# Kernel tuning notes

Measured on AMD Instinct MI355X. Metric: run time of the kernel, lower is better.

The kernel has to match this reference:

```python
import jax, jax.numpy as jnp
import numpy as np

B, N, K = 8, 1024, 32
C_IN, C_OUT, C_SIPF, HEADS = 128, 256, 8, 4
D_H = C_IN // HEADS
EPS = 1e-5
NEG_SLOPE = 0.2


def setup_inputs() -> dict:
    key = jax.random.key(0)
    ks = jax.random.split(key, 12)
    s = 0.05
    x = jax.random.normal(ks[0], (B, C_IN, N), jnp.float32)
    SiPF = jax.random.normal(ks[1], (B, N, K, C_SIPF), jnp.float32)
    col_local = jax.random.randint(ks[2], (B, N, K), 0, N)
    # feat_select expects GLOBAL indices (it subtracts the b*N base)
    col = (col_local + jnp.arange(B)[:, None, None] * N).reshape(-1).astype(jnp.int64)
    return {
        "x": x,
        "SiPF": SiPF,
        "w_kv": jax.random.normal(ks[3], (2 * C_IN, C_IN), jnp.float32) * s,
        "wk1": jax.random.normal(ks[4], (C_IN, C_SIPF), jnp.float32) * s,
        "bnk_gamma": jnp.ones((C_IN,), jnp.float32),
        "bnk_beta": jnp.zeros((C_IN,), jnp.float32),
        "wk2": jax.random.normal(ks[5], (C_IN, C_IN), jnp.float32) * s,
        "wv1": jax.random.normal(ks[6], (C_IN, C_SIPF), jnp.float32) * s,
        "bv1": jnp.zeros((C_IN,), jnp.float32),
        "bnv_gamma": jnp.ones((C_IN,), jnp.float32),
        "bnv_beta": jnp.zeros((C_IN,), jnp.float32),
        "wv2": jax.random.normal(ks[7], (C_IN, C_IN), jnp.float32) * s,
        "bv2": jnp.zeros((C_IN,), jnp.float32),
        "we": jax.random.normal(ks[8], (C_OUT, 2 * C_IN), jnp.float32) * s,
        "bne_gamma": jnp.ones((C_OUT,), jnp.float32),
        "bne_beta": jnp.zeros((C_OUT,), jnp.float32),
        "col": col,
        "bs": B,
    }


def _bn2d(t, gamma, beta):
    # BatchNorm2d, training mode: stats over (B, N, K) per channel
    m = t.mean(axis=(0, 2, 3), keepdims=True)
    v = t.var(axis=(0, 2, 3), keepdims=True)
    return (t - m) * jax.lax.rsqrt(v + EPS) * gamma[None, :, None, None] + beta[None, :, None, None]


def _bn1d(t, gamma, beta):
    m = t.mean(axis=(0, 2), keepdims=True)
    v = t.var(axis=(0, 2), keepdims=True)
    return (t - m) * jax.lax.rsqrt(v + EPS) * gamma[None, :, None] + beta[None, :, None]


def _feat_select(feat, col):
    # feat: [B, C, N]; col: [B*N*K] global indices -> [B, C, N, K]
    idx = col.reshape(B, N * K) - (jnp.arange(B, dtype=col.dtype) * N)[:, None]
    gathered = jax.vmap(lambda f, i: f[:, i])(feat, idx)  # [B, C, N*K]
    return gathered.reshape(feat.shape[0], feat.shape[1], N, K)


def _forward(x, SiPF, col, w_kv, wk1, bnk_gamma, bnk_beta, wk2,
             wv1, bv1, bnv_gamma, bnv_beta, wv2, bv2, we, bne_gamma, bne_beta):
    fs = _feat_select(x, col)                               # [B, C_in, N, K]
    sipf = SiPF.reshape(B, N, K, C_SIPF).transpose(0, 3, 1, 2)  # [B, C_sipf, N, K]

    qv = jnp.einsum('oc,bcnk->bonk', w_kv, fs)
    q_fs, v_fs = qv[:, :C_IN], qv[:, C_IN:]

    # bias nets on SiPF (1x1 conv -> BN -> ReLU -> 1x1 conv)
    hk = jax.nn.relu(_bn2d(jnp.einsum('oc,bcnk->bonk', wk1, sipf), bnk_gamma, bnk_beta))
    k_sipf = jnp.einsum('oc,bcnk->bonk', wk2, hk)
    hv = jnp.einsum('oc,bcnk->bonk', wv1, sipf) + bv1[None, :, None, None]
    hv = jax.nn.relu(_bn2d(hv, bnv_gamma, bnv_beta))
    v_sipf = jnp.einsum('oc,bcnk->bonk', wv2, hv) + bv2[None, :, None, None]

    def to_heads(t):  # [B, C_in, N, K] -> [B, H, N, K, d_h]
        return t.reshape(B, HEADS, D_H, N, K).transpose(0, 1, 3, 4, 2)

    q = to_heads(q_fs)
    k = to_heads(k_sipf)
    v = to_heads(v_fs) * to_heads(v_sipf)

    scale = 1.0 / np.sqrt(D_H).astype(np.float32)
    scores = jnp.einsum('bhnkd,bhnjd->bhnkj', q, k) * scale   # [B, H, N, K, K]
    attn = jax.nn.softmax(scores, axis=-1)
    out = jnp.einsum('bhnkj,bhnjd->bhnkd', attn, v)           # [B, H, N, K, d_h]

    y = out.transpose(0, 1, 4, 2, 3).reshape(B, C_IN, N, K)
    y = y.max(axis=-1)                                        # [B, C_in, N]

    z = jnp.concatenate([y - x, x], axis=1)                   # [B, 2*C_in, N]
    z = jnp.einsum('oc,bcn->bon', we, z)
    z = _bn1d(z, bne_gamma, bne_beta)
    return jnp.where(z >= 0, z, NEG_SLOPE * z)                # LeakyReLU(0.2)


def reference(x, SiPF, w_kv, wk1, bnk_gamma, bnk_beta, wk2, wv1, bv1,
              bnv_gamma, bnv_beta, wv2, bv2, we, bne_gamma, bne_beta, col, bs):
    del bs  # unused by the torch module as well
    return _forward(x, SiPF, col, w_kv, wk1, bnk_gamma, bnk_beta, wk2,
                    wv1, bv1, bnv_gamma, bnv_beta, wv2, bv2, we, bne_gamma, bne_beta)
```

## Files before the change

### kernel.cpp

```cpp
#include <hip/hip_runtime.h>

#define B_    8
#define N_    1024
#define K_    32
#define CIN   128
#define COUT  256
#define EPSF  1e-5f
#define NEG   0.2f

#define WS_MP   0
#define WS_ESUM 12288
#define WS_ESS  12544
#define WS_BK   12800
#define WS_BV   12928
#define WB_BYTE 53248
#define XT_BYTE 331776
#define Y_BYTE  2428928
#define WQB   0
#define WVB   16384
#define WK2B  32768
#define WV2B  49152
#define WEB   65536
#define WK1F  131072
#define WV1F  135168

typedef unsigned short ushort_t;
typedef unsigned int   uint_t;
typedef __attribute__((ext_vector_type(8))) short s8v;
typedef __attribute__((ext_vector_type(4))) short s4v;
typedef __attribute__((ext_vector_type(4))) float f4v;
typedef __bf16 bf16x8 __attribute__((ext_vector_type(8)));

constexpr int   P_TOT  = B_ * N_ * K_;
constexpr float INV_P  = 1.0f / (float)P_TOT;
constexpr float INV_BN = 1.0f / (float)(B_ * N_);

__device__ __forceinline__ float b2f(ushort_t u) {
    return __uint_as_float(((uint_t)u) << 16);
}
__device__ __forceinline__ ushort_t f2b(float f) {
    return __builtin_bit_cast(ushort_t, (__bf16)f);
}
__device__ __forceinline__ bf16x8 ld8(const ushort_t* p) {
    return __builtin_bit_cast(bf16x8, *(const s8v*)p);
}
__device__ __forceinline__ int qx2(int c, int k) {
    return (c * 32 + k) ^ (((c >> 1) & 7) << 3);
}

__global__ __launch_bounds__(256) void prep_kernel(
    const float* __restrict__ x, const float* __restrict__ SiPF,
    const float* __restrict__ w_kv, const float* __restrict__ wk2,
    const float* __restrict__ wv2, const float* __restrict__ we,
    float* __restrict__ ws, ushort_t* __restrict__ wb,
    ushort_t* __restrict__ xT)
{
    __shared__ float red[4][44];
    __shared__ float tile[32][129];
    const int blk = blockIdx.x;
    const int t   = threadIdx.x;

    if (blk < 256) {
        float s1[8], s2[36];
#pragma unroll
        for (int i = 0; i < 8; ++i) s1[i] = 0.f;
#pragma unroll
        for (int i = 0; i < 36; ++i) s2[i] = 0.f;
        const int tid = blk * 256 + t;
#pragma unroll
        for (int it = 0; it < P_TOT / 65536; ++it) {
            const float4* base = (const float4*)(SiPF + (size_t)(tid + it * 65536) * 8);
            float4 a = base[0], bq = base[1];
            float v[8] = {a.x, a.y, a.z, a.w, bq.x, bq.y, bq.z, bq.w};
            int idx = 0;
#pragma unroll
            for (int i = 0; i < 8; ++i) {
                s1[i] += v[i];
#pragma unroll
                for (int j = i; j < 8; ++j) s2[idx++] += v[i] * v[j];
            }
        }
#pragma unroll
        for (int i = 0; i < 8; ++i)
            for (int m = 32; m; m >>= 1) s1[i] += __shfl_xor(s1[i], m);
#pragma unroll
        for (int i = 0; i < 36; ++i)
            for (int m = 32; m; m >>= 1) s2[i] += __shfl_xor(s2[i], m);
        if ((t & 63) == 0) {
            const int w = t >> 6;
#pragma unroll
            for (int i = 0; i < 8; ++i) red[w][i] = s1[i];
#pragma unroll
            for (int i = 0; i < 36; ++i) red[w][8 + i] = s2[i];
        }
        __syncthreads();
        if (t < 44)
            ws[WS_MP + blk * 48 + t] = red[0][t] + red[1][t] + red[2][t] + red[3][t];
    } else if (blk < 512) {
        const int tb = blk - 256;
        const int b  = tb >> 5;
        const int n0 = (tb & 31) << 5;
        const int cgr = t >> 5, n = t & 31;
#pragma unroll
        for (int i = 0; i < 16; ++i) {
            const int c = cgr * 16 + i;
            tile[n][c] = x[((size_t)(b * CIN + c)) * N_ + n0 + n];
        }
        __syncthreads();
        const int nr = t >> 3, c0 = (t & 7) * 16;
        s8v o0, o1;
#pragma unroll
        for (int j = 0; j < 8; ++j) {
            o0[j] = (short)f2b(tile[nr][c0 + j]);
            o1[j] = (short)f2b(tile[nr][c0 + 8 + j]);
        }
        s8v* dst = (s8v*)(xT + ((size_t)(b * N_ + n0 + nr)) * 128 + c0);
        dst[0] = o0; dst[1] = o1;
    } else {
        if (blk == 512) {
            ws[WS_ESUM + t] = 0.f;
            ws[WS_ESS + t]  = 0.f;
        }
        const int base = (blk - 512) * 1024 + t;
#pragma unroll
        for (int i = 0; i < 4; ++i) {
            const int e = base + i * 256;
            float v;
            if (e < 32768)      v = w_kv[e];
            else if (e < 49152) v = wk2[e - 32768];
            else if (e < 65536) v = wv2[e - 49152];
            else                v = we[e - 65536];
            wb[e] = f2b(v);
        }
    }
}

__global__ __launch_bounds__(128) void prep2_kernel(
    const float* __restrict__ wk1, const float* __restrict__ wv1,
    const float* __restrict__ bnk_gamma, const float* __restrict__ bnk_beta,
    const float* __restrict__ bnv_gamma, const float* __restrict__ bnv_beta,
    float* __restrict__ ws, ushort_t* __restrict__ wb)
{
    __shared__ float red2[44];
    const int c = threadIdx.x;
    if (c < 44) {
        float s = 0.f;
        for (int bq = 0; bq < 256; ++bq) s += ws[WS_MP + bq * 48 + c];
        red2[c] = s;
    }
    __syncthreads();

    float m1[8], wkr[8], wvr[8];
#pragma unroll
    for (int s = 0; s < 8; ++s) {
        m1[s]  = red2[s] * INV_P;
        wkr[s] = wk1[c * 8 + s];
        wvr[s] = wv1[c * 8 + s];
    }
    float mk = 0.f, mv = 0.f;
#pragma unroll
    for (int s = 0; s < 8; ++s) { mk += wkr[s] * m1[s]; mv += wvr[s] * m1[s]; }
    float ek = 0.f, ev = 0.f;
#pragma unroll
    for (int s = 0; s < 8; ++s)
#pragma unroll
        for (int s2 = 0; s2 < 8; ++s2) {
            const int i = s < s2 ? s : s2;
            const int j = s < s2 ? s2 : s;
            const float m2 = red2[8 + 8 * i - (i * (i - 1)) / 2 + (j - i)] * INV_P;
            ek += wkr[s] * wkr[s2] * m2;
            ev += wvr[s] * wvr[s2] * m2;
        }
    const float Ak = bnk_gamma[c] * rsqrtf(ek - mk * mk + EPSF);
    const float Av = bnv_gamma[c] * rsqrtf(ev - mv * mv + EPSF);
    ws[WS_BK + c] = bnk_beta[c] - mk * Ak;
    ws[WS_BV + c] = bnv_beta[c] - mv * Av;
#pragma unroll
    for (int s = 0; s < 32; ++s) {
        wb[WK1F + c * 32 + s] = s < 8 ? f2b(Ak * wkr[s]) : (ushort_t)0;
        wb[WV1F + c * 32 + s] = s < 8 ? f2b(Av * wvr[s]) : (ushort_t)0;
    }
}

__global__ __launch_bounds__(512, 4) void main_kernel(
    const float* __restrict__ SiPF, const float* __restrict__ bv2,
    const int* __restrict__ col,    const float* __restrict__ ws,
    const ushort_t* __restrict__ wb, const ushort_t* __restrict__ xT,
    ushort_t* __restrict__ y)
{
    __shared__ __align__(16) ushort_t T1[2][4096];
    __shared__ __align__(16) ushort_t T2[2][4096];
    __shared__ __align__(16) ushort_t T3[2][4096];
    __shared__ __align__(16) ushort_t T4[2][4096];

    const int bid = blockIdx.x;
    const int pi  = (bid & 7) * 512 + (bid >> 3);
    const int t   = threadIdx.x;

    {
        const int p  = t >> 8;
        const int bn = pi * 2 + p;
        const int b  = bn >> 10;
        const int tt = t & 255;
        const int k  = tt & 31;
        const int cg = tt >> 5;
        if (cg < 4) {
            const int slot = (cg * 8) ^ ((k & 3) << 3);
            s8v o8 = {0, 0, 0, 0, 0, 0, 0, 0};
            if (cg == 0) {
                const float4* sp = (const float4*)(SiPF + (size_t)bn * 256 + k * 8);
                const float4 sa = sp[0], sq = sp[1];
                o8[0] = (short)f2b(sa.x); o8[1] = (short)f2b(sa.y);
                o8[2] = (short)f2b(sa.z); o8[3] = (short)f2b(sa.w);
                o8[4] = (short)f2b(sq.x); o8[5] = (short)f2b(sq.y);
                o8[6] = (short)f2b(sq.z); o8[7] = (short)f2b(sq.w);
            }
            *(s8v*)&T4[p][k * 32 + slot] = o8;
        }
        const int idxk = col[bn * K_ + k] - b * N_;
        const s8v* xrow = (const s8v*)(xT + ((size_t)(b << 10) + idxk) * 128 + cg * 16);
        const s8v f0 = xrow[0], f1 = xrow[1];
        const int base = k * 128 + cg * 16;
        const int sw   = (k & 7) << 3;
        *(s8v*)&T1[p][(base) ^ sw]     = f0;
        *(s8v*)&T1[p][(base + 8) ^ sw] = f1;
    }
    __syncthreads();

    const int wv_ = t >> 6, l = t & 63, lr = l & 15, lg = l >> 4;
    const int cw  = wv_ * 16;
    const f4v z4 = {0.f, 0.f, 0.f, 0.f};

    {
        bf16x8 sb[4];
#pragma unroll
        for (int nt = 0; nt < 4; ++nt) {
            const int pp  = nt >> 1;
            const int row = (nt & 1) * 16 + lr;
            sb[nt] = ld8(&T4[pp][row * 32 + ((lg * 8) ^ ((row & 3) << 3))]);
        }
        const float4 bka = *(const float4*)&ws[WS_BK + cw + lg * 4];
        const float4 bva = *(const float4*)&ws[WS_BV + cw + lg * 4];
        const float Bk_[4] = {bka.x, bka.y, bka.z, bka.w};
        const float Bv_[4] = {bva.x, bva.y, bva.z, bva.w};
        const bf16x8 a1 = ld8(&wb[WK1F + (cw + lr) * 32 + lg * 8]);
        const bf16x8 a2 = ld8(&wb[WV1F + (cw + lr) * 32 + lg * 8]);
        f4v hka[4], hva[4];
#pragma unroll
        for (int nt = 0; nt < 4; ++nt) {
            hka[nt] = __builtin_amdgcn_mfma_f32_16x16x32_bf16(a1, sb[nt], z4, 0, 0, 0);
            hva[nt] = __builtin_amdgcn_mfma_f32_16x16x32_bf16(a2, sb[nt], z4, 0, 0, 0);
        }
#pragma unroll
        for (int nt = 0; nt < 4; ++nt) {
            const int pp  = nt >> 1;
            const int c0  = cw + lg * 4;
            const int kc  = (nt & 1) * 16 + lr;
            const int idx = (kc * 128 + c0) ^ ((kc & 7) << 3);
            s4v hk4, hv4;
#pragma unroll
            for (int r = 0; r < 4; ++r) {
                hk4[r] = (short)f2b(fmaxf(hka[nt][r] + Bk_[r], 0.f));
                hv4[r] = (short)f2b(fmaxf(hva[nt][r] + Bv_[r], 0.f));
            }
            *(s4v*)&T2[pp][idx] = hk4;
            *(s4v*)&T3[pp][idx] = hv4;
        }
    }
    __syncthreads();

    f4v ck[4], cs[4], aq[4], av[4];
#pragma unroll
    for (int nt = 0; nt < 4; ++nt) { ck[nt] = z4; cs[nt] = z4; aq[nt] = z4; av[nt] = z4; }
    __builtin_amdgcn_s_setprio(1);
#pragma unroll
    for (int kt = 0; kt < 4; ++kt) {
        const int cp0 = kt * 32 + lg * 8;
        bf16x8 bk[4], bv[4], bfr[4];
#pragma unroll
        for (int nt = 0; nt < 4; ++nt) {
            const int pp  = nt >> 1;
            const int kk_ = (nt & 1) * 16 + lr;
            const int idx = (kk_ * 128 + cp0) ^ ((lr & 7) << 3);
            bk[nt]  = ld8(&T2[pp][idx]);
            bv[nt]  = ld8(&T3[pp][idx]);
            bfr[nt] = ld8(&T1[pp][idx]);
        }
        const int c = cw + lr;
        const bf16x8 a1 = ld8(&wb[WK2B + c * 128 + cp0]);
        const bf16x8 a2 = ld8(&wb[WV2B + c * 128 + cp0]);
        const bf16x8 a3 = ld8(&wb[WQB  + c * 128 + cp0]);
        const bf16x8 a4 = ld8(&wb[WVB  + c * 128 + cp0]);
#pragma unroll
        for (int nt = 0; nt < 4; ++nt) {
            ck[nt] = __builtin_amdgcn_mfma_f32_16x16x32_bf16(a1, bk[nt],  ck[nt], 0, 0, 0);
            cs[nt] = __builtin_amdgcn_mfma_f32_16x16x32_bf16(a2, bv[nt],  cs[nt], 0, 0, 0);
            aq[nt] = __builtin_amdgcn_mfma_f32_16x16x32_bf16(a3, bfr[nt], aq[nt], 0, 0, 0);
            av[nt] = __builtin_amdgcn_mfma_f32_16x16x32_bf16(a4, bfr[nt], av[nt], 0, 0, 0);
        }
    }
    __builtin_amdgcn_s_setprio(0);
#pragma unroll
    for (int nt = 0; nt < 4; ++nt) {
        const int pp  = nt >> 1;
        const int c0  = cw + lg * 4;
        const int kk_ = (nt & 1) * 16 + lr;
        const int idx = (kk_ * 128 + c0) ^ ((kk_ & 7) << 3);
        s4v ck4;
#pragma unroll
        for (int r = 0; r < 4; ++r) ck4[r] = (short)f2b(ck[nt][r]);
        *(s4v*)&T4[pp][idx] = ck4;
    }
    __syncthreads();

    {
        const float4 bvv = *(const float4*)&bv2[cw + lg * 4];
        const float bv2_[4] = {bvv.x, bvv.y, bvv.z, bvv.w};
        const float SC = 0.17677669529663687f;
#pragma unroll
        for (int nt = 0; nt < 4; ++nt) {
            const int pp  = nt >> 1;
            const int c0  = cw + lg * 4;
            const int kk_ = (nt & 1) * 16 + lr;
            const int idx = (kk_ * 128 + c0) ^ ((kk_ & 7) << 3);
            s4v q4;
#pragma unroll
            for (int r = 0; r < 4; ++r) {
                q4[r] = (short)f2b(aq[nt][r] * SC);
                T3[pp][qx2(c0 + r, kk_)] =
                    f2b(av[nt][r] * (cs[nt][r] + bv2_[r]));
            }
            *(s4v*)&T2[pp][idx] = q4;
        }
    }
    __syncthreads();

    {
        const int pp = wv_ >> 2;
        const int h  = wv_ & 3;
        const int bn = pi * 2 + pp;
        bf16x8 aqf[2], bkf[2];
#pragma unroll
        for (int mt = 0; mt < 2; ++mt)
            aqf[mt] = ld8(&T2[pp][((mt * 16 + lr) * 128 + h * 32 + lg * 8) ^ ((lr & 7) << 3)]);
#pragma unroll
        for (int nt = 0; nt < 2; ++nt)
            bkf[nt] = ld8(&T4[pp][((nt * 16 + lr) * 128 + h * 32 + lg * 8) ^ ((lr & 7) << 3)]);
        f4v s[2][2];
#pragma unroll
        for (int mt = 0; mt < 2; ++mt)
#pragma unroll
            for (int nt = 0; nt < 2; ++nt)
                s[mt][nt] = __builtin_amdgcn_mfma_f32_16x16x32_bf16(aqf[mt], bkf[nt], z4, 0, 0, 0);

        ushort_t* P = &T1[pp][h * 1024];
#pragma unroll
        for (int mt = 0; mt < 2; ++mt)
#pragma unroll
            for (int nt = 0; nt < 2; ++nt) {
                const int kq0 = mt * 16 + lg * 4;
                const int j   = nt * 16 + lr;
#pragma unroll
                for (int r = 0; r < 4; ++r) {
                    const int kq = kq0 + r;
                    P[(kq * 32 + j) ^ ((kq & 7) << 3)] = f2b(__expf(s[mt][nt][r]));
                }
            }

        bf16x8 af[2], pb[2];
#pragma unroll
        for (int mt2 = 0; mt2 < 2; ++mt2)
            af[mt2] = ld8(&T3[pp][qx2(h * 32 + mt2 * 16 + lr, lg * 8)]);
#pragma unroll
        for (int nt2 = 0; nt2 < 2; ++nt2) {
            const int kq2 = nt2 * 16 + lr;
            pb[nt2] = ld8(&P[(kq2 * 32 + lg * 8) ^ ((lr & 7) << 3)]);
        }
        const s8v one8 = {(short)0x3F80, (short)0x3F80, (short)0x3F80, (short)0x3F80,
                          (short)0x3F80, (short)0x3F80, (short)0x3F80, (short)0x3F80};
        const bf16x8 ones = __builtin_bit_cast(bf16x8, one8);

        f4v o2[2][2], rsf[2];
        __builtin_amdgcn_s_setprio(1);
#pragma unroll
        for (int mt2 = 0; mt2 < 2; ++mt2)
#pragma unroll
            for (int nt2 = 0; nt2 < 2; ++nt2)
                o2[mt2][nt2] = __builtin_amdgcn_mfma_f32_16x16x32_bf16(af[mt2], pb[nt2], z4, 0, 0, 0);
#pragma unroll
        for (int nt2 = 0; nt2 < 2; ++nt2)
            rsf[nt2] = __builtin_amdgcn_mfma_f32_16x16x32_bf16(ones, pb[nt2], z4, 0, 0, 0);
        __builtin_amdgcn_s_setprio(0);

        const float inv0 = 1.0f / rsf[0][0];
        const float inv1 = 1.0f / rsf[1][0];

        float ym[2][4];
#pragma unroll
        for (int mt2 = 0; mt2 < 2; ++mt2)
#pragma unroll
            for (int r = 0; r < 4; ++r)
                ym[mt2][r] = fmaxf(o2[mt2][0][r] * inv0, o2[mt2][1][r] * inv1);
#pragma unroll
        for (int m = 1; m <= 8; m <<= 1)
#pragma unroll
            for (int mt2 = 0; mt2 < 2; ++mt2)
#pragma unroll
                for (int r = 0; r < 4; ++r)
                    ym[mt2][r] = fmaxf(ym[mt2][r], __shfl_xor(ym[mt2][r], m));
        if (lr == 0) {
#pragma unroll
            for (int mt2 = 0; mt2 < 2; ++mt2) {
                unsigned long long pk = 0;
#pragma unroll
                for (int r = 0; r < 4; ++r)
                    pk |= ((unsigned long long)f2b(ym[mt2][r])) << (16 * r);
                *(unsigned long long*)&y[(size_t)bn * 128 + h * 32 + mt2 * 16 + lg * 4] = pk;
            }
        }
    }
}

__global__ __launch_bounds__(256) void zgemm_kernel(
    const ushort_t* __restrict__ wb, const ushort_t* __restrict__ xT,
    const ushort_t* __restrict__ y, float* __restrict__ ws,
    float* __restrict__ out)
{
    __shared__ __align__(16) ushort_t Bt[32 * 256];
    const int blk = blockIdx.x;
    const int bn0 = (blk >> 1) * 32;
    const int mh  = (blk & 1) * 128;
    const int t   = threadIdx.x;
    {
        const int r   = t >> 3;
        const int c0  = (t & 7) * 16;
        const int bnr = bn0 + r;
        const s8v* yr = (const s8v*)(y  + (size_t)bnr * 128 + c0);
        const s8v* xr = (const s8v*)(xT + (size_t)bnr * 128 + c0);
        const s8v y0 = yr[0], y1 = yr[1], x0 = xr[0], x1 = xr[1];
        s8v d0, d1;
#pragma unroll
        for (int j = 0; j < 8; ++j) {
            d0[j] = (short)f2b(b2f((ushort_t)y0[j]) - b2f((ushort_t)x0[j]));
            d1[j] = (short)f2b(b2f((ushort_t)y1[j]) - b2f((ushort_t)x1[j]));
        }
        const int sw = (r & 7) << 3;
        *(s8v*)&Bt[(r * 256 + c0) ^ sw]           = d0;
        *(s8v*)&Bt[(r * 256 + c0 + 8) ^ sw]       = d1;
        *(s8v*)&Bt[(r * 256 + 128 + c0) ^ sw]     = x0;
        *(s8v*)&Bt[(r * 256 + 128 + c0 + 8) ^ sw] = x1;
    }
    __syncthreads();

    const int w = t >> 6, l = t & 63, lr = l & 15, lg = l >> 4;
    const f4v z4 = {0.f, 0.f, 0.f, 0.f};
    f4v acc[2][2];
#pragma unroll
    for (int mt = 0; mt < 2; ++mt)
#pragma unroll
        for (int nt = 0; nt < 2; ++nt) acc[mt][nt] = z4;

#pragma unroll
    for (int kt = 0; kt < 8; ++kt) {
        const int kc = kt * 32 + lg * 8;
        bf16x8 bf[2];
#pragma unroll
        for (int nt = 0; nt < 2; ++nt) {
            const int rl = nt * 16 + lr;
            bf[nt] = ld8(&Bt[(rl * 256 + kc) ^ ((lr & 7) << 3)]);
        }
#pragma unroll
        for (int mt = 0; mt < 2; ++mt) {
            const int o = mh + w * 32 + mt * 16 + lr;
            const bf16x8 am = ld8(&wb[WEB + o * 256 + kc]);
#pragma unroll
            for (int nt = 0; nt < 2; ++nt)
                acc[mt][nt] = __builtin_amdgcn_mfma_f32_16x16x32_bf16(am, bf[nt], acc[mt][nt], 0, 0, 0);
        }
    }

    float sm[2][4], sq[2][4];
#pragma unroll
    for (int mt = 0; mt < 2; ++mt)
#pragma unroll
        for (int r = 0; r < 4; ++r) {
            const float a0 = acc[mt][0][r], a1 = acc[mt][1][r];
            sm[mt][r] = a0 + a1;
            sq[mt][r] = a0 * a0 + a1 * a1;
        }
#pragma unroll
    for (int m = 1; m <= 8; m <<= 1)
#pragma unroll
        for (int mt = 0; mt < 2; ++mt)
#pragma unroll
            for (int r = 0; r < 4; ++r) {
                sm[mt][r] += __shfl_xor(sm[mt][r], m);
                sq[mt][r] += __shfl_xor(sq[mt][r], m);
            }
    if (lr == 0) {
#pragma unroll
        for (int mt = 0; mt < 2; ++mt)
#pragma unroll
            for (int r = 0; r < 4; ++r) {
                const int o = mh + w * 32 + mt * 16 + lg * 4 + r;
                atomicAdd(&ws[WS_ESUM + o], sm[mt][r]);
                atomicAdd(&ws[WS_ESS + o],  sq[mt][r]);
            }
    }
    const int b = bn0 >> 10;
#pragma unroll
    for (int mt = 0; mt < 2; ++mt)
#pragma unroll
        for (int r = 0; r < 4; ++r) {
            const int o = mh + w * 32 + mt * 16 + lg * 4 + r;
#pragma unroll
            for (int nt = 0; nt < 2; ++nt) {
                const int n = (bn0 + nt * 16 + lr) & (N_ - 1);
                out[((size_t)(b * COUT + o)) * N_ + n] = acc[mt][nt][r];
            }
        }
}

__global__ __launch_bounds__(256) void apply_kernel(
    const float* __restrict__ ws, const float* __restrict__ gamma,
    const float* __restrict__ beta, float* __restrict__ out)
{
    const int bo = blockIdx.x;
    const int o  = bo & 255;
    const int b  = bo >> 8;
    const float mean = ws[WS_ESUM + o] * INV_BN;
    const float var  = ws[WS_ESS + o] * INV_BN - mean * mean;
    const float A  = gamma[o] * rsqrtf(var + EPSF);
    const float Bb = beta[o] - mean * A;
    float4* p = (float4*)(out + ((size_t)(b * COUT + o)) * N_);
    float4 v = p[threadIdx.x];
    float r0 = A * v.x + Bb, r1 = A * v.y + Bb;
    float r2 = A * v.z + Bb, r3 = A * v.w + Bb;
    v.x = r0 >= 0.f ? r0 : NEG * r0;
    v.y = r1 >= 0.f ? r1 : NEG * r1;
    v.z = r2 >= 0.f ? r2 : NEG * r2;
    v.w = r3 >= 0.f ? r3 : NEG * r3;
    p[threadIdx.x] = v;
}

extern "C" void kernel_launch(void* const* d_in, const int* in_sizes, int n_in,
                              void* d_out, int out_size, void* d_ws, size_t ws_size,
                              hipStream_t stream)
{
    (void)in_sizes; (void)n_in; (void)out_size; (void)ws_size;

    const float* x         = (const float*)d_in[0];
    const float* SiPF      = (const float*)d_in[1];
    const float* w_kv      = (const float*)d_in[2];
    const float* wk1       = (const float*)d_in[3];
    const float* bnk_gamma = (const float*)d_in[4];
    const float* bnk_beta  = (const float*)d_in[5];
    const float* wk2       = (const float*)d_in[6];
    const float* wv1       = (const float*)d_in[7];
    const float* bnv_gamma = (const float*)d_in[9];
    const float* bnv_beta  = (const float*)d_in[10];
    const float* wv2       = (const float*)d_in[11];
    const float* bv2       = (const float*)d_in[12];
    const float* we        = (const float*)d_in[13];
    const float* bne_gamma = (const float*)d_in[14];
    const float* bne_beta  = (const float*)d_in[15];
    const int*   col       = (const int*)d_in[16];

    float*    ws = (float*)d_ws;
    ushort_t* wb = (ushort_t*)((char*)d_ws + WB_BYTE);
    ushort_t* xT = (ushort_t*)((char*)d_ws + XT_BYTE);
    ushort_t* y  = (ushort_t*)((char*)d_ws + Y_BYTE);

    prep_kernel<<<640, 256, 0, stream>>>(x, SiPF, w_kv, wk2, wv2, we, ws, wb, xT);
    prep2_kernel<<<1, 128, 0, stream>>>(wk1, wv1, bnk_gamma, bnk_beta,
                                        bnv_gamma, bnv_beta, ws, wb);
    main_kernel<<<4096, 512, 0, stream>>>(SiPF, bv2, col, ws, wb, xT, y);
    zgemm_kernel<<<512, 256, 0, stream>>>(wb, xT, y, ws, (float*)d_out);
    apply_kernel<<<2048, 256, 0, stream>>>(ws, bne_gamma, bne_beta,
                                           (float*)d_out);
}
```

Before: 159.1 us.

## Make main kernel loop over 8 point pairs with register prefetch of next gather

The main kernel now launches 512 blocks instead of 4096, and each block loops over 8 consecutive point pairs. During the compute phase of the current pair, the gathered x rows and SiPF for the next pair are loaded into registers, so global gather latency overlaps with the MFMA work. To make the T1 buffer free for the next iteration's stores, the softmax probabilities now go to T2, which adds one extra barrier per iteration plus an end-of-iteration barrier. Block-to-point mapping changes from the XCD-interleaved order to contiguous ranges. The lower block count (about 2 blocks per CU) reduces occupancy and latency hiding across waves.

```diff
diff --git a/kernel.cpp b/kernel.cpp
--- a/kernel.cpp
+++ b/kernel.cpp
@@ -194,230 +194,253 @@
     __shared__ __align__(16) ushort_t T4[2][4096];
 
     const int bid = blockIdx.x;
-    const int pi  = (bid & 7) * 512 + (bid >> 3);
     const int t   = threadIdx.x;
-
+    const int wv_ = t >> 6, l = t & 63, lr = l & 15, lg = l >> 4;
+    const int cw  = wv_ * 16;
+    const int p   = t >> 8;
+    const int tt  = t & 255, k = tt & 31, cg = tt >> 5;
+    const f4v z4 = {0.f, 0.f, 0.f, 0.f};
+
+    s8v    f0n, f1n;
+    float4 sp0n = {0,0,0,0}, sp1n = {0,0,0,0};
     {
-        const int p  = t >> 8;
-        const int bn = pi * 2 + p;
-        const int b  = bn >> 10;
-        const int tt = t & 255;
-        const int k  = tt & 31;
-        const int cg = tt >> 5;
-        if (cg < 4) {
-            const int slot = (cg * 8) ^ ((k & 3) << 3);
-            s8v o8 = {0, 0, 0, 0, 0, 0, 0, 0};
-            if (cg == 0) {
-                const float4* sp = (const float4*)(SiPF + (size_t)bn * 256 + k * 8);
-                const float4 sa = sp[0], sq = sp[1];
-                o8[0] = (short)f2b(sa.x); o8[1] = (short)f2b(sa.y);
-                o8[2] = (short)f2b(sa.z); o8[3] = (short)f2b(sa.w);
-                o8[4] = (short)f2b(sq.x); o8[5] = (short)f2b(sq.y);
-                o8[6] = (short)f2b(sq.z); o8[7] = (short)f2b(sq.w);
-            }
-            *(s8v*)&T4[p][k * 32 + slot] = o8;
-        }
+        const int bn   = bid * 16 + p;
+        const int b    = bn >> 10;
         const int idxk = col[bn * K_ + k] - b * N_;
         const s8v* xrow = (const s8v*)(xT + ((size_t)(b << 10) + idxk) * 128 + cg * 16);
-        const s8v f0 = xrow[0], f1 = xrow[1];
-        const int base = k * 128 + cg * 16;
-        const int sw   = (k & 7) << 3;
-        *(s8v*)&T1[p][(base) ^ sw]     = f0;
-        *(s8v*)&T1[p][(base + 8) ^ sw] = f1;
-    }
-    __syncthreads();
-
-    const int wv_ = t >> 6, l = t & 63, lr = l & 15, lg = l >> 4;
-    const int cw  = wv_ * 16;
-    const f4v z4 = {0.f, 0.f, 0.f, 0.f};
-
-    {
-        bf16x8 sb[4];
-#pragma unroll
-        for (int nt = 0; nt < 4; ++nt) {
-            const int pp  = nt >> 1;
-            const int row = (nt & 1) * 16 + lr;
-            sb[nt] = ld8(&T4[pp][row * 32 + ((lg * 8) ^ ((row & 3) << 3))]);
-        }
-        const float4 bka = *(const float4*)&ws[WS_BK + cw + lg * 4];
-        const float4 bva = *(const float4*)&ws[WS_BV + cw + lg * 4];
-        const float Bk_[4] = {bka.x, bka.y, bka.z, bka.w};
-        const float Bv_[4] = {bva.x, bva.y, bva.z, bva.w};
-        const bf16x8 a1 = ld8(&wb[WK1F + (cw + lr) * 32 + lg * 8]);
-        const bf16x8 a2 = ld8(&wb[WV1F + (cw + lr) * 32 + lg * 8]);
-        f4v hka[4], hva[4];
-#pragma unroll
-        for (int nt = 0; nt < 4; ++nt) {
-            hka[nt] = __builtin_amdgcn_mfma_f32_16x16x32_bf16(a1, sb[nt], z4, 0, 0, 0);
-            hva[nt] = __builtin_amdgcn_mfma_f32_16x16x32_bf16(a2, sb[nt], z4, 0, 0, 0);
-        }
-#pragma unroll
-        for (int nt = 0; nt < 4; ++nt) {
-            const int pp  = nt >> 1;
-            const int c0  = cw + lg * 4;
-            const int kc  = (nt & 1) * 16 + lr;
-            const int idx = (kc * 128 + c0) ^ ((kc & 7) << 3);
-            s4v hk4, hv4;
-#pragma unroll
-            for (int r = 0; r < 4; ++r) {
-                hk4[r] = (short)f2b(fmaxf(hka[nt][r] + Bk_[r], 0.f));
-                hv4[r] = (short)f2b(fmaxf(hva[nt][r] + Bv_[r], 0.f));
-            }
-            *(s4v*)&T2[pp][idx] = hk4;
-            *(s4v*)&T3[pp][idx] = hv4;
-        }
-    }
-    __syncthreads();
-
-    f4v ck[4], cs[4], aq[4], av[4];
-#pragma unroll
-    for (int nt = 0; nt < 4; ++nt) { ck[nt] = z4; cs[nt] = z4; aq[nt] = z4; av[nt] = z4; }
-    __builtin_amdgcn_s_setprio(1);
-#pragma unroll
-    for (int kt = 0; kt < 4; ++kt) {
-        const int cp0 = kt * 32 + lg * 8;
-        bf16x8 bk[4], bv[4], bfr[4];
-#pragma unroll
-        for (int nt = 0; nt < 4; ++nt) {
-            const int pp  = nt >> 1;
-            const int kk_ = (nt & 1) * 16 + lr;
-            const int idx = (kk_ * 128 + cp0) ^ ((lr & 7) << 3);
-            bk[nt]  = ld8(&T2[pp][idx]);
-            bv[nt]  = ld8(&T3[pp][idx]);
-            bfr[nt] = ld8(&T1[pp][idx]);
-        }
-        const int c = cw + lr;
-        const bf16x8 a1 = ld8(&wb[WK2B + c * 128 + cp0]);
-        const bf16x8 a2 = ld8(&wb[WV2B + c * 128 + cp0]);
-        const bf16x8 a3 = ld8(&wb[WQB  + c * 128 + cp0]);
-        const bf16x8 a4 = ld8(&wb[WVB  + c * 128 + cp0]);
-#pragma unroll
-        for (int nt = 0; nt < 4; ++nt) {
-            ck[nt] = __builtin_amdgcn_mfma_f32_16x16x32_bf16(a1, bk[nt],  ck[nt], 0, 0, 0);
-            cs[nt] = __builtin_amdgcn_mfma_f32_16x16x32_bf16(a2, bv[nt],  cs[nt], 0, 0, 0);
-            aq[nt] = __builtin_amdgcn_mfma_f32_16x16x32_bf16(a3, bfr[nt], aq[nt], 0, 0, 0);
-            av[nt] = __builtin_amdgcn_mfma_f32_16x16x32_bf16(a4, bfr[nt], av[nt], 0, 0, 0);
-        }
-    }
-    __builtin_amdgcn_s_setprio(0);
-#pragma unroll
-    for (int nt = 0; nt < 4; ++nt) {
-        const int pp  = nt >> 1;
-        const int c0  = cw + lg * 4;
-        const int kk_ = (nt & 1) * 16 + lr;
-        const int idx = (kk_ * 128 + c0) ^ ((kk_ & 7) << 3);
-        s4v ck4;
-#pragma unroll
-        for (int r = 0; r < 4; ++r) ck4[r] = (short)f2b(ck[nt][r]);
-        *(s4v*)&T4[pp][idx] = ck4;
-    }
-    __syncthreads();
-
-    {
-        const float4 bvv = *(const float4*)&bv2[cw + lg * 4];
-        const float bv2_[4] = {bvv.x, bvv.y, bvv.z, bvv.w};
-        const float SC = 0.17677669529663687f;
+        f0n = xrow[0]; f1n = xrow[1];
+        if (cg == 0) {
+            const float4* sp = (const float4*)(SiPF + (size_t)bn * 256 + k * 8);
+            sp0n = sp[0]; sp1n = sp[1];
+        }
+    }
+
+    for (int it = 0; it < 8; ++it) {
+        const int pi = bid * 8 + it;
+
+        {
+            const int base = k * 128 + cg * 16;
+            const int sw   = (k & 7) << 3;
+            *(s8v*)&T1[p][(base) ^ sw]     = f0n;
+            *(s8v*)&T1[p][(base + 8) ^ sw] = f1n;
+            if (cg < 4) {
+                const int slot = (cg * 8) ^ ((k & 3) << 3);
+                s8v o8 = {0, 0, 0, 0, 0, 0, 0, 0};
+                if (cg == 0) {
+                    o8[0] = (short)f2b(sp0n.x); o8[1] = (short)f2b(sp0n.y);
+                    o8[2] = (short)f2b(sp0n.z); o8[3] = (short)f2b(sp0n.w);
+                    o8[4] = (short)f2b(sp1n.x); o8[5] = (short)f2b(sp1n.y);
+                    o8[6] = (short)f2b(sp1n.z); o8[7] = (short)f2b(sp1n.w);
+                }
+                *(s8v*)&T4[p][k * 32 + slot] = o8;
+            }
+        }
+        __syncthreads();
+
+        {
+            bf16x8 sb[4];
+#pragma unroll
+            for (int nt = 0; nt < 4; ++nt) {
+                const int pp  = nt >> 1;
+                const int row = (nt & 1) * 16 + lr;
+                sb[nt] = ld8(&T4[pp][row * 32 + ((lg * 8) ^ ((row & 3) << 3))]);
+            }
+            const float4 bka = *(const float4*)&ws[WS_BK + cw + lg * 4];
+            const float4 bva = *(const float4*)&ws[WS_BV + cw + lg * 4];
+            const float Bk_[4] = {bka.x, bka.y, bka.z, bka.w};
+            const float Bv_[4] = {bva.x, bva.y, bva.z, bva.w};
+            const bf16x8 a1 = ld8(&wb[WK1F + (cw + lr) * 32 + lg * 8]);
+            const bf16x8 a2 = ld8(&wb[WV1F + (cw + lr) * 32 + lg * 8]);
+            f4v hka[4], hva[4];
+#pragma unroll
+            for (int nt = 0; nt < 4; ++nt) {
+                hka[nt] = __builtin_amdgcn_mfma_f32_16x16x32_bf16(a1, sb[nt], z4, 0, 0, 0);
+                hva[nt] = __builtin_amdgcn_mfma_f32_16x16x32_bf16(a2, sb[nt], z4, 0, 0, 0);
+            }
+#pragma unroll
+            for (int nt = 0; nt < 4; ++nt) {
+                const int pp  = nt >> 1;
+                const int c0  = cw + lg * 4;
+                const int kc  = (nt & 1) * 16 + lr;
+                const int idx = (kc * 128 + c0) ^ ((kc & 7) << 3);
+                s4v hk4, hv4;
+#pragma unroll
+                for (int r = 0; r < 4; ++r) {
+                    hk4[r] = (short)f2b(fmaxf(hka[nt][r] + Bk_[r], 0.f));
+                    hv4[r] = (short)f2b(fmaxf(hva[nt][r] + Bv_[r], 0.f));
+                }
+                *(s4v*)&T2[pp][idx] = hk4;
+                *(s4v*)&T3[pp][idx] = hv4;
+            }
+        }
+        __syncthreads();
+
+        f4v ck[4], cs[4], aq[4], av[4];
+#pragma unroll
+        for (int nt = 0; nt < 4; ++nt) { ck[nt] = z4; cs[nt] = z4; aq[nt] = z4; av[nt] = z4; }
+        __builtin_amdgcn_s_setprio(1);
+#pragma unroll
+        for (int kt = 0; kt < 4; ++kt) {
+            const int cp0 = kt * 32 + lg * 8;
+            bf16x8 bk[4], bv[4], bfr[4];
+#pragma unroll
+            for (int nt = 0; nt < 4; ++nt) {
+                const int pp  = nt >> 1;
+                const int kk_ = (nt & 1) * 16 + lr;
+                const int idx = (kk_ * 128 + cp0) ^ ((lr & 7) << 3);
+                bk[nt]  = ld8(&T2[pp][idx]);
+                bv[nt]  = ld8(&T3[pp][idx]);
+                bfr[nt] = ld8(&T1[pp][idx]);
+            }
+            const int c = cw + lr;
+            const bf16x8 a1 = ld8(&wb[WK2B + c * 128 + cp0]);
+            const bf16x8 a2 = ld8(&wb[WV2B + c * 128 + cp0]);
+            const bf16x8 a3 = ld8(&wb[WQB  + c * 128 + cp0]);
+            const bf16x8 a4 = ld8(&wb[WVB  + c * 128 + cp0]);
+#pragma unroll
+            for (int nt = 0; nt < 4; ++nt) {
+                ck[nt] = __builtin_amdgcn_mfma_f32_16x16x32_bf16(a1, bk[nt],  ck[nt], 0, 0, 0);
+                cs[nt] = __builtin_amdgcn_mfma_f32_16x16x32_bf16(a2, bv[nt],  cs[nt], 0, 0, 0);
+                aq[nt] = __builtin_amdgcn_mfma_f32_16x16x32_bf16(a3, bfr[nt], aq[nt], 0, 0, 0);
+                av[nt] = __builtin_amdgcn_mfma_f32_16x16x32_bf16(a4, bfr[nt], av[nt], 0, 0, 0);
+            }
+        }
+        __builtin_amdgcn_s_setprio(0);
+
+        if (it < 7) {
+            const int bnn  = (pi + 1) * 2 + p;
+            const int bb   = bnn >> 10;
+            const int idxn = col[bnn * K_ + k] - bb * N_;
+            const s8v* xr2 = (const s8v*)(xT + ((size_t)(bb << 10) + idxn) * 128 + cg * 16);
+            f0n = xr2[0]; f1n = xr2[1];
+            if (cg == 0) {
+                const float4* sp = (const float4*)(SiPF + (size_t)bnn * 256 + k * 8);
+                sp0n = sp[0]; sp1n = sp[1];
+            }
+        }
+
 #pragma unroll
         for (int nt = 0; nt < 4; ++nt) {
             const int pp  = nt >> 1;
             const int c0  = cw + lg * 4;
             const int kk_ = (nt & 1) * 16 + lr;
             const int idx = (kk_ * 128 + c0) ^ ((kk_ & 7) << 3);
-            s4v q4;
-#pragma unroll
-            for (int r = 0; r < 4; ++r) {
-                q4[r] = (short)f2b(aq[nt][r] * SC);
-                T3[pp][qx2(c0 + r, kk_)] =
-                    f2b(av[nt][r] * (cs[nt][r] + bv2_[r]));
-            }
-            *(s4v*)&T2[pp][idx] = q4;
-        }
-    }
-    __syncthreads();
-
-    {
-        const int pp = wv_ >> 2;
-        const int h  = wv_ & 3;
-        const int bn = pi * 2 + pp;
-        bf16x8 aqf[2], bkf[2];
-#pragma unroll
-        for (int mt = 0; mt < 2; ++mt)
-            aqf[mt] = ld8(&T2[pp][((mt * 16 + lr) * 128 + h * 32 + lg * 8) ^ ((lr & 7) << 3)]);
-#pragma unroll
-        for (int nt = 0; nt < 2; ++nt)
-            bkf[nt] = ld8(&T4[pp][((nt * 16 + lr) * 128 + h * 32 + lg * 8) ^ ((lr & 7) << 3)]);
-        f4v s[2][2];
-#pragma unroll
-        for (int mt = 0; mt < 2; ++mt)
+            s4v ck4;
+#pragma unroll
+            for (int r = 0; r < 4; ++r) ck4[r] = (short)f2b(ck[nt][r]);
+            *(s4v*)&T4[pp][idx] = ck4;
+        }
+        __syncthreads();
+
+        {
+            const float4 bvv = *(const float4*)&bv2[cw + lg * 4];
+            const float bv2_[4] = {bvv.x, bvv.y, bvv.z, bvv.w};
+            const float SC = 0.17677669529663687f;
+#pragma unroll
+            for (int nt = 0; nt < 4; ++nt) {
+                const int pp  = nt >> 1;
+                const int c0  = cw + lg * 4;
+                const int kk_ = (nt & 1) * 16 + lr;
+                const int idx = (kk_ * 128 + c0) ^ ((kk_ & 7) << 3);
+                s4v q4;
+#pragma unroll
+                for (int r = 0; r < 4; ++r) {
+                    q4[r] = (short)f2b(aq[nt][r] * SC);
+                    T3[pp][qx2(c0 + r, kk_)] =
+                        f2b(av[nt][r] * (cs[nt][r] + bv2_[r]));
+                }
+                *(s4v*)&T2[pp][idx] = q4;
+            }
+        }
+        __syncthreads();
+
+        {
+            const int pp = wv_ >> 2;
+            const int h  = wv_ & 3;
+            const int bn = pi * 2 + pp;
+            bf16x8 aqf[2], bkf[2];
+#pragma unroll
+            for (int mt = 0; mt < 2; ++mt)
+                aqf[mt] = ld8(&T2[pp][((mt * 16 + lr) * 128 + h * 32 + lg * 8) ^ ((lr & 7) << 3)]);
 #pragma unroll
             for (int nt = 0; nt < 2; ++nt)
-                s[mt][nt] = __builtin_amdgcn_mfma_f32_16x16x32_bf16(aqf[mt], bkf[nt], z4, 0, 0, 0);
-
-        ushort_t* P = &T1[pp][h * 1024];
-#pragma unroll
-        for (int mt = 0; mt < 2; ++mt)
-#pragma unroll
-            for (int nt = 0; nt < 2; ++nt) {
-                const int kq0 = mt * 16 + lg * 4;
-                const int j   = nt * 16 + lr;
-#pragma unroll
-                for (int r = 0; r < 4; ++r) {
-                    const int kq = kq0 + r;
-                    P[(kq * 32 + j) ^ ((kq & 7) << 3)] = f2b(__expf(s[mt][nt][r]));
+                bkf[nt] = ld8(&T4[pp][((nt * 16 + lr) * 128 + h * 32 + lg * 8) ^ ((lr & 7) << 3)]);
+            f4v s[2][2];
+#pragma unroll
+            for (int mt = 0; mt < 2; ++mt)
+#pragma unroll
+                for (int nt = 0; nt < 2; ++nt)
+                    s[mt][nt] = __builtin_amdgcn_mfma_f32_16x16x32_bf16(aqf[mt], bkf[nt], z4, 0, 0, 0);
+
+            __syncthreads();
+
+            ushort_t* P = &T2[pp][h * 1024];
+#pragma unroll
+            for (int mt = 0; mt < 2; ++mt)
+#pragma unroll
+                for (int nt = 0; nt < 2; ++nt) {
+                    const int kq0 = mt * 16 + lg * 4;
+                    const int j   = nt * 16 + lr;
+#pragma unroll
+                    for (int r = 0; r < 4; ++r) {
+                        const int kq = kq0 + r;
+                        P[(kq * 32 + j) ^ ((kq & 7) << 3)] = f2b(__expf(s[mt][nt][r]));
+                    }
                 }
-            }
-
-        bf16x8 af[2], pb[2];
-#pragma unroll
-        for (int mt2 = 0; mt2 < 2; ++mt2)
-            af[mt2] = ld8(&T3[pp][qx2(h * 32 + mt2 * 16 + lr, lg * 8)]);
-#pragma unroll
-        for (int nt2 = 0; nt2 < 2; ++nt2) {
-            const int kq2 = nt2 * 16 + lr;
-            pb[nt2] = ld8(&P[(kq2 * 32 + lg * 8) ^ ((lr & 7) << 3)]);
-        }
-        const s8v one8 = {(short)0x3F80, (short)0x3F80, (short)0x3F80, (short)0x3F80,
-                          (short)0x3F80, (short)0x3F80, (short)0x3F80, (short)0x3F80};
-        const bf16x8 ones = __builtin_bit_cast(bf16x8, one8);
-
-        f4v o2[2][2], rsf[2];
-        __builtin_amdgcn_s_setprio(1);
-#pragma unroll
-        for (int mt2 = 0; mt2 < 2; ++mt2)
+
+            bf16x8 af[2], pb[2];
+#pragma unroll
+            for (int mt2 = 0; mt2 < 2; ++mt2)
+                af[mt2] = ld8(&T3[pp][qx2(h * 32 + mt2 * 16 + lr, lg * 8)]);
+#pragma unroll
+            for (int nt2 = 0; nt2 < 2; ++nt2) {
+                const int kq2 = nt2 * 16 + lr;
+                pb[nt2] = ld8(&P[(kq2 * 32 + lg * 8) ^ ((lr & 7) << 3)]);
+            }
+            const s8v one8 = {(short)0x3F80, (short)0x3F80, (short)0x3F80, (short)0x3F80,
+                              (short)0x3F80, (short)0x3F80, (short)0x3F80, (short)0x3F80};
+            const bf16x8 ones = __builtin_bit_cast(bf16x8, one8);
+
+            f4v o2[2][2], rsf[2];
+            __builtin_amdgcn_s_setprio(1);
+#pragma unroll
+            for (int mt2 = 0; mt2 < 2; ++mt2)
+#pragma unroll
+                for (int nt2 = 0; nt2 < 2; ++nt2)
+                    o2[mt2][nt2] = __builtin_amdgcn_mfma_f32_16x16x32_bf16(af[mt2], pb[nt2], z4, 0, 0, 0);
 #pragma unroll
             for (int nt2 = 0; nt2 < 2; ++nt2)
-                o2[mt2][nt2] = __builtin_amdgcn_mfma_f32_16x16x32_bf16(af[mt2], pb[nt2], z4, 0, 0, 0);
-#pragma unroll
-        for (int nt2 = 0; nt2 < 2; ++nt2)
-            rsf[nt2] = __builtin_amdgcn_mfma_f32_16x16x32_bf16(ones, pb[nt2], z4, 0, 0, 0);
-        __builtin_amdgcn_s_setprio(0);
-
-        const float inv0 = 1.0f / rsf[0][0];
-        const float inv1 = 1.0f / rsf[1][0];
-
-        float ym[2][4];
-#pragma unroll
-        for (int mt2 = 0; mt2 < 2; ++mt2)
-#pragma unroll
-            for (int r = 0; r < 4; ++r)
-                ym[mt2][r] = fmaxf(o2[mt2][0][r] * inv0, o2[mt2][1][r] * inv1);
-#pragma unroll
-        for (int m = 1; m <= 8; m <<= 1)
+                rsf[nt2] = __builtin_amdgcn_mfma_f32_16x16x32_bf16(ones, pb[nt2], z4, 0, 0, 0);
+            __builtin_amdgcn_s_setprio(0);
+
+            const float inv0 = 1.0f / rsf[0][0];
+            const float inv1 = 1.0f / rsf[1][0];
+
+            float ym[2][4];
 #pragma unroll
             for (int mt2 = 0; mt2 < 2; ++mt2)
 #pragma unroll
                 for (int r = 0; r < 4; ++r)
-                    ym[mt2][r] = fmaxf(ym[mt2][r], __shfl_xor(ym[mt2][r], m));
-        if (lr == 0) {
-#pragma unroll
-            for (int mt2 = 0; mt2 < 2; ++mt2) {
-                unsigned long long pk = 0;
-#pragma unroll
-                for (int r = 0; r < 4; ++r)
-                    pk |= ((unsigned long long)f2b(ym[mt2][r])) << (16 * r);
-                *(unsigned long long*)&y[(size_t)bn * 128 + h * 32 + mt2 * 16 + lg * 4] = pk;
-            }
-        }
+                    ym[mt2][r] = fmaxf(o2[mt2][0][r] * inv0, o2[mt2][1][r] * inv1);
+#pragma unroll
+            for (int m = 1; m <= 8; m <<= 1)
+#pragma unroll
+                for (int mt2 = 0; mt2 < 2; ++mt2)
+#pragma unroll
+                    for (int r = 0; r < 4; ++r)
+                        ym[mt2][r] = fmaxf(ym[mt2][r], __shfl_xor(ym[mt2][r], m));
+            if (lr == 0) {
+#pragma unroll
+                for (int mt2 = 0; mt2 < 2; ++mt2) {
+                    unsigned long long pk = 0;
+#pragma unroll
+                    for (int r = 0; r < 4; ++r)
+                        pk |= ((unsigned long long)f2b(ym[mt2][r])) << (16 * r);
+                    *(unsigned long long*)&y[(size_t)bn * 128 + h * 32 + mt2 * 16 + lg * 4] = pk;
+                }
+            }
+        }
+        __syncthreads();
     }
 }
 
@@ -574,7 +597,7 @@
     prep_kernel<<<640, 256, 0, stream>>>(x, SiPF, w_kv, wk2, wv2, we, ws, wb, xT);
     prep2_kernel<<<1, 128, 0, stream>>>(wk1, wv1, bnk_gamma, bnk_beta,
                                         bnv_gamma, bnv_beta, ws, wb);
-    main_kernel<<<4096, 512, 0, stream>>>(SiPF, bv2, col, ws, wb, xT, y);
+    main_kernel<<<512, 512, 0, stream>>>(SiPF, bv2, col, ws, wb, xT, y);
     zgemm_kernel<<<512, 256, 0, stream>>>(wb, xT, y, ws, (float*)d_out);
     apply_kernel<<<2048, 256, 0, stream>>>(ws, bne_gamma, bne_beta,
                                            (float*)d_out);
```

Result: slower. 288.9 us (+81.6%).

## Fuse BN-apply into zgemm via cooperative grid sync, halve tile size

Applied to the files above, without the earlier changes.

Merges the final batch-norm apply and LeakyReLU pass into the z GEMM kernel. The kernel is now launched cooperatively with a grid-wide barrier after the statistics atomics, so each block normalizes its own accumulators and writes the output once. This removes the separate apply kernel and its extra read and write of the output. Tiles shrink to 16 columns so 1024 blocks can all be resident at once. The risk is the cost of the grid sync and the co-residency requirement of the cooperative launch.

```diff
diff --git a/kernel.cpp b/kernel.cpp
--- a/kernel.cpp
+++ b/kernel.cpp
@@ -1,4 +1,6 @@
 #include <hip/hip_runtime.h>
+#include <hip/hip_cooperative_groups.h>
+namespace cg = cooperative_groups;
 
 #define B_    8
 #define N_    1024
@@ -421,61 +423,58 @@
     }
 }
 
-__global__ __launch_bounds__(256) void zgemm_kernel(
+__global__ __launch_bounds__(256, 4) void zgemm_kernel(
     const ushort_t* __restrict__ wb, const ushort_t* __restrict__ xT,
     const ushort_t* __restrict__ y, float* __restrict__ ws,
+    const float* __restrict__ gamma, const float* __restrict__ beta,
     float* __restrict__ out)
 {
-    __shared__ __align__(16) ushort_t Bt[32 * 256];
+    __shared__ __align__(16) ushort_t Bt[16 * 256];
     const int blk = blockIdx.x;
-    const int bn0 = (blk >> 1) * 32;
+    const int bn0 = (blk >> 1) * 16;
     const int mh  = (blk & 1) * 128;
     const int t   = threadIdx.x;
     {
-        const int r   = t >> 3;
-        const int c0  = (t & 7) * 16;
+        const int r   = t >> 4;
+        const int c0  = (t & 15) * 16;
         const int bnr = bn0 + r;
-        const s8v* yr = (const s8v*)(y  + (size_t)bnr * 128 + c0);
-        const s8v* xr = (const s8v*)(xT + (size_t)bnr * 128 + c0);
-        const s8v y0 = yr[0], y1 = yr[1], x0 = xr[0], x1 = xr[1];
-        s8v d0, d1;
-#pragma unroll
-        for (int j = 0; j < 8; ++j) {
-            d0[j] = (short)f2b(b2f((ushort_t)y0[j]) - b2f((ushort_t)x0[j]));
-            d1[j] = (short)f2b(b2f((ushort_t)y1[j]) - b2f((ushort_t)x1[j]));
-        }
-        const int sw = (r & 7) << 3;
-        *(s8v*)&Bt[(r * 256 + c0) ^ sw]           = d0;
-        *(s8v*)&Bt[(r * 256 + c0 + 8) ^ sw]       = d1;
-        *(s8v*)&Bt[(r * 256 + 128 + c0) ^ sw]     = x0;
-        *(s8v*)&Bt[(r * 256 + 128 + c0 + 8) ^ sw] = x1;
+        const int sw  = (r & 7) << 3;
+        if (c0 < 128) {
+            const s8v y0 = *(const s8v*)(y  + (size_t)bnr * 128 + c0);
+            const s8v x0 = *(const s8v*)(xT + (size_t)bnr * 128 + c0);
+            const s8v y1 = *(const s8v*)(y  + (size_t)bnr * 128 + c0 + 8);
+            const s8v x1 = *(const s8v*)(xT + (size_t)bnr * 128 + c0 + 8);
+            s8v d0, d1;
+#pragma unroll
+            for (int j = 0; j < 8; ++j) {
+                d0[j] = (short)f2b(b2f((ushort_t)y0[j]) - b2f((ushort_t)x0[j]));
+                d1[j] = (short)f2b(b2f((ushort_t)y1[j]) - b2f((ushort_t)x1[j]));
+            }
+            *(s8v*)&Bt[(r * 256 + c0) ^ sw]     = d0;
+            *(s8v*)&Bt[(r * 256 + c0 + 8) ^ sw] = d1;
+        } else {
+            const s8v x0 = *(const s8v*)(xT + (size_t)bnr * 128 + (c0 - 128));
+            const s8v x1 = *(const s8v*)(xT + (size_t)bnr * 128 + (c0 - 128) + 8);
+            *(s8v*)&Bt[(r * 256 + c0) ^ sw]     = x0;
+            *(s8v*)&Bt[(r * 256 + c0 + 8) ^ sw] = x1;
+        }
     }
     __syncthreads();
 
     const int w = t >> 6, l = t & 63, lr = l & 15, lg = l >> 4;
     const f4v z4 = {0.f, 0.f, 0.f, 0.f};
-    f4v acc[2][2];
-#pragma unroll
-    for (int mt = 0; mt < 2; ++mt)
-#pragma unroll
-        for (int nt = 0; nt < 2; ++nt) acc[mt][nt] = z4;
+    f4v acc[2];
+    acc[0] = z4; acc[1] = z4;
 
 #pragma unroll
     for (int kt = 0; kt < 8; ++kt) {
         const int kc = kt * 32 + lg * 8;
-        bf16x8 bf[2];
-#pragma unroll
-        for (int nt = 0; nt < 2; ++nt) {
-            const int rl = nt * 16 + lr;
-            bf[nt] = ld8(&Bt[(rl * 256 + kc) ^ ((lr & 7) << 3)]);
-        }
+        const bf16x8 bf = ld8(&Bt[(lr * 256 + kc) ^ ((lr & 7) << 3)]);
 #pragma unroll
         for (int mt = 0; mt < 2; ++mt) {
             const int o = mh + w * 32 + mt * 16 + lr;
             const bf16x8 am = ld8(&wb[WEB + o * 256 + kc]);
-#pragma unroll
-            for (int nt = 0; nt < 2; ++nt)
-                acc[mt][nt] = __builtin_amdgcn_mfma_f32_16x16x32_bf16(am, bf[nt], acc[mt][nt], 0, 0, 0);
+            acc[mt] = __builtin_amdgcn_mfma_f32_16x16x32_bf16(am, bf, acc[mt], 0, 0, 0);
         }
     }
 
@@ -484,9 +483,9 @@
     for (int mt = 0; mt < 2; ++mt)
 #pragma unroll
         for (int r = 0; r < 4; ++r) {
-            const float a0 = acc[mt][0][r], a1 = acc[mt][1][r];
-            sm[mt][r] = a0 + a1;
-            sq[mt][r] = a0 * a0 + a1 * a1;
+            const float a0 = acc[mt][r];
+            sm[mt][r] = a0;
+            sq[mt][r] = a0 * a0;
         }
 #pragma unroll
     for (int m = 1; m <= 8; m <<= 1)
@@ -507,40 +506,23 @@
                 atomicAdd(&ws[WS_ESS + o],  sq[mt][r]);
             }
     }
+
+    cg::this_grid().sync();
+
     const int b = bn0 >> 10;
 #pragma unroll
     for (int mt = 0; mt < 2; ++mt)
 #pragma unroll
         for (int r = 0; r < 4; ++r) {
             const int o = mh + w * 32 + mt * 16 + lg * 4 + r;
-#pragma unroll
-            for (int nt = 0; nt < 2; ++nt) {
-                const int n = (bn0 + nt * 16 + lr) & (N_ - 1);
-                out[((size_t)(b * COUT + o)) * N_ + n] = acc[mt][nt][r];
-            }
-        }
-}
-
-__global__ __launch_bounds__(256) void apply_kernel(
-    const float* __restrict__ ws, const float* __restrict__ gamma,
-    const float* __restrict__ beta, float* __restrict__ out)
-{
-    const int bo = blockIdx.x;
-    const int o  = bo & 255;
-    const int b  = bo >> 8;
-    const float mean = ws[WS_ESUM + o] * INV_BN;
-    const float var  = ws[WS_ESS + o] * INV_BN - mean * mean;
-    const float A  = gamma[o] * rsqrtf(var + EPSF);
-    const float Bb = beta[o] - mean * A;
-    float4* p = (float4*)(out + ((size_t)(b * COUT + o)) * N_);
-    float4 v = p[threadIdx.x];
-    float r0 = A * v.x + Bb, r1 = A * v.y + Bb;
-    float r2 = A * v.z + Bb, r3 = A * v.w + Bb;
-    v.x = r0 >= 0.f ? r0 : NEG * r0;
-    v.y = r1 >= 0.f ? r1 : NEG * r1;
-    v.z = r2 >= 0.f ? r2 : NEG * r2;
-    v.w = r3 >= 0.f ? r3 : NEG * r3;
-    p[threadIdx.x] = v;
+            const float mean = ws[WS_ESUM + o] * INV_BN;
+            const float var  = ws[WS_ESS + o] * INV_BN - mean * mean;
+            const float A  = gamma[o] * rsqrtf(var + EPSF);
+            const float Bb = beta[o] - mean * A;
+            const int n = (bn0 + lr) & (N_ - 1);
+            const float rv = A * acc[mt][r] + Bb;
+            out[((size_t)(b * COUT + o)) * N_ + n] = rv >= 0.f ? rv : NEG * rv;
+        }
 }
 
 extern "C" void kernel_launch(void* const* d_in, const int* in_sizes, int n_in,
@@ -570,12 +552,15 @@
     ushort_t* wb = (ushort_t*)((char*)d_ws + WB_BYTE);
     ushort_t* xT = (ushort_t*)((char*)d_ws + XT_BYTE);
     ushort_t* y  = (ushort_t*)((char*)d_ws + Y_BYTE);
+    float*    outp = (float*)d_out;
 
     prep_kernel<<<640, 256, 0, stream>>>(x, SiPF, w_kv, wk2, wv2, we, ws, wb, xT);
     prep2_kernel<<<1, 128, 0, stream>>>(wk1, wv1, bnk_gamma, bnk_beta,
                                         bnv_gamma, bnv_beta, ws, wb);
     main_kernel<<<4096, 512, 0, stream>>>(SiPF, bv2, col, ws, wb, xT, y);
-    zgemm_kernel<<<512, 256, 0, stream>>>(wb, xT, y, ws, (float*)d_out);
-    apply_kernel<<<2048, 256, 0, stream>>>(ws, bne_gamma, bne_beta,
-                                           (float*)d_out);
-}
+
+    void* zargs[] = {(void*)&wb, (void*)&xT, (void*)&y, (void*)&ws,
+                     (void*)&bne_gamma, (void*)&bne_beta, (void*)&outp};
+    hipLaunchCooperativeKernel((const void*)zgemm_kernel, dim3(1024), dim3(256),
+                               zargs, 0, stream);
+}
```

New measurement: 261.3 us. 64.3% more time.
